# Optimization experiments

Measured on AMD Instinct MI355X. Metric: run time of the kernel, lower is better.

Reference implementation:

```python
import jax, jax.numpy as jnp
import numpy as np

N_EMBED = 512
E_DIM = 256
BETA = 0.25


def setup_inputs() -> dict:
    key = jax.random.key(0)
    k1, k2 = jax.random.split(key)
    z = jax.random.normal(k1, (32, 16, 16, 16, E_DIM), dtype=jnp.float32)
    embedding = jax.random.normal(k2, (N_EMBED, E_DIM), dtype=jnp.float32)
    return {"z": z, "embedding": embedding}


def reference(z, embedding):
    # Flatten spatial/batch dims: [N, e_dim]
    zf = z.reshape(-1, E_DIM)
    # similarity = ||z||^2 + ||e||^2 - 2 z.e  (squared distances)
    sim = (
        jnp.sum(zf * zf, axis=1, keepdims=True)
        + jnp.sum(embedding * embedding, axis=1)
        - 2.0 * jnp.einsum("bd,nd->bn", zf, embedding)
    )
    # NOTE: original code uses argmax (farthest code) -- faithfully reproduced.
    codebook_idxs = jnp.argmax(sim, axis=-1)
    # histogram side-effect: codebook_hist[idx] += 1
    hist = jnp.zeros((N_EMBED,), dtype=jnp.float32).at[codebook_idxs].add(1.0)
    z_q = embedding[codebook_idxs].reshape(z.shape)
    vq_loss = jnp.mean((z_q - jax.lax.stop_gradient(z)) ** 2)
    commitment_loss = BETA * jnp.mean((jax.lax.stop_gradient(z_q) - z) ** 2)
    # straight-through estimator
    z_q_st = z + jax.lax.stop_gradient(z_q - z)
    return (z_q_st, vq_loss, commitment_loss, codebook_idxs, hist)
```

## Files before the change

kernel.cpp:

```cpp
#include <hip/hip_runtime.h>
#include <hip/hip_bf16.h>

#define D 256
#define NC 512
#define NROWS 131072L

#define OFF_ZQ   0L
#define OFF_VQ   33554432L
#define OFF_CM   33554433L
#define OFF_IDX  33554434L
#define OFF_HIST 33685506L

#define WS_LPART 0
#define WS_HIST  2048
#define WS_E2    2560
#define WS_CNT   3072
#define WS_AMB   3136
#define WS_FIDX  134208
#define WS_BK    265280
#define WS_NEED  (330816L * 4)

#define MARGIN 1.25f

typedef __attribute__((ext_vector_type(8))) short bf16x8;
typedef __attribute__((ext_vector_type(4))) float f32x4;

#define AS1 __attribute__((address_space(1)))
#define AS3 __attribute__((address_space(3)))

__device__ __forceinline__ unsigned short f2bf(float f) {
    union { float f; unsigned int u; } a; a.f = f;
    return (unsigned short)((a.u + 0x7FFFu + ((a.u >> 16) & 1u)) >> 16);
}

__global__ void vq_init(float* __restrict__ ws) {
    int i = blockIdx.x * 1024 + threadIdx.x;
    if (i < 3073) ws[i] = 0.0f;
}

__global__ void vq_e2(const float* __restrict__ e, float* __restrict__ e2) {
    int c = blockIdx.x;
    int l = threadIdx.x;
    float4 v = *(const float4*)(e + c * D + l * 4);
    float s = v.x * v.x + v.y * v.y + v.z * v.z + v.w * v.w;
    #pragma unroll
    for (int off = 32; off; off >>= 1) s += __shfl_xor(s, off);
    if (l == 0) e2[c] = s;
}

__global__ void vq_convB(const float* __restrict__ e, unsigned short* __restrict__ Bk) {
    int code = blockIdx.x, k = threadIdx.x;
    unsigned short h = f2bf(e[code * D + k]);
    Bk[((k >> 5) * NC + code) * 32 + (k & 31)] = h;
}

__global__ __launch_bounds__(512, 4)
void vq_gemm(const float* __restrict__ z, const unsigned short* __restrict__ Bk,
             const float* __restrict__ e2, int* __restrict__ fidx,
             int* __restrict__ acnt, int* __restrict__ alist) {
    __shared__ __align__(16) unsigned short zh[64 * 264];
    __shared__ __align__(16) unsigned short Bs[512 * 32];
    __shared__ float red[64 * 4 * 3];

    const int tid = threadIdx.x;
    const int w = tid >> 6, l = tid & 63, q = l >> 4, ln = l & 15;
    const int wm = w >> 2, wn = w & 3;
    const long row0 = (long)blockIdx.x * 64;

    #pragma unroll
    for (int j = 0; j < 8; ++j) {
        int c = j * 512 + tid;
        int row = c >> 6, c4 = (c & 63) * 4;
        float4 av = *(const float4*)(z + (row0 + row) * D + c4);
        *(ushort4*)&zh[row * 264 + c4] =
            make_ushort4(f2bf(av.x), f2bf(av.y), f2bf(av.z), f2bf(av.w));
    }

    int bidx[8];
    #pragma unroll
    for (int nt = 0; nt < 8; ++nt) {
        int code = wn * 128 + nt * 16 + ln;
        int c = code * 4 + q;
        int d = c ^ ((code >> 1) & 3);
        bidx[nt] = d * 8;
    }

    f32x4 acc[2][8];
    #pragma unroll
    for (int mt = 0; mt < 2; ++mt)
        #pragma unroll
        for (int nt = 0; nt < 8; ++nt) acc[mt][nt] = (f32x4){0.f, 0.f, 0.f, 0.f};

    for (int s = 0; s < 8; ++s) {
        __syncthreads();
        const unsigned short* slabB = Bk + s * (NC * 32);
        #pragma unroll
        for (int j = 0; j < 4; ++j) {
            int dd = j * 512 + tid;
            int cc = dd ^ ((dd >> 3) & 3);
            __builtin_amdgcn_global_load_lds((const AS1 void*)(slabB + cc * 8),
                                             (AS3 void*)(Bs + dd * 8), 16, 0, 0);
        }
        __syncthreads();
        bf16x8 af[2], bfr[8];
        #pragma unroll
        for (int mt = 0; mt < 2; ++mt)
            af[mt] = *(const bf16x8*)&zh[(wm * 32 + mt * 16 + ln) * 264 + s * 32 + q * 8];
        #pragma unroll
        for (int nt = 0; nt < 8; ++nt)
            bfr[nt] = *(const bf16x8*)&Bs[bidx[nt]];
        #pragma unroll
        for (int mt = 0; mt < 2; ++mt)
            #pragma unroll
            for (int nt = 0; nt < 8; ++nt)
                acc[mt][nt] = __builtin_amdgcn_mfma_f32_16x16x32_bf16(af[mt], bfr[nt], acc[mt][nt], 0, 0, 0);
    }

    float e2v[8];
    #pragma unroll
    for (int nt = 0; nt < 8; ++nt) e2v[nt] = e2[wn * 128 + nt * 16 + ln];

    #pragma unroll
    for (int mt = 0; mt < 2; ++mt) {
        #pragma unroll
        for (int r = 0; r < 4; ++r) {
            float v1 = -3.0e38f, v2 = -3.0e38f; int i1 = 0;
            #pragma unroll
            for (int nt = 0; nt < 8; ++nt) {
                float v = e2v[nt] - 2.0f * acc[mt][nt][r];
                int c = wn * 128 + nt * 16 + ln;
                if (v > v1) { v2 = v1; v1 = v; i1 = c; }
                else if (v > v2) v2 = v;
            }
            #pragma unroll
            for (int off = 1; off < 16; off <<= 1) {
                float ov1 = __shfl_xor(v1, off);
                float ov2 = __shfl_xor(v2, off);
                int   oi1 = __shfl_xor(i1, off);
                if (ov1 > v1 || (ov1 == v1 && oi1 < i1)) {
                    v2 = fmaxf(v1, ov2); v1 = ov1; i1 = oi1;
                } else {
                    v2 = fmaxf(v2, ov1);
                }
            }
            if (ln == 0) {
                int rr = wm * 32 + mt * 16 + q * 4 + r;
                red[rr * 12 + wn * 3 + 0] = v1;
                red[rr * 12 + wn * 3 + 1] = (float)i1;
                red[rr * 12 + wn * 3 + 2] = v2;
            }
        }
    }
    __syncthreads();
    if (tid < 64) {
        float v1 = -3.0e38f, v2 = -3.0e38f; int i1 = 0;
        #pragma unroll
        for (int g = 0; g < 4; ++g) {
            float rv1 = red[tid * 12 + g * 3 + 0];
            int   ri  = (int)red[tid * 12 + g * 3 + 1];
            float rv2 = red[tid * 12 + g * 3 + 2];
            if (rv1 > v1) { v2 = fmaxf(v1, rv2); v1 = rv1; i1 = ri; }
            else v2 = fmaxf(v2, rv1);
        }
        fidx[row0 + tid] = i1;
        if (v1 - v2 < MARGIN) {
            int ppos = atomicAdd(acnt, 1);
            alist[ppos] = (int)(row0 + tid);
        }
    }
}

__global__ __launch_bounds__(256, 2)
void vq_refine(const float* __restrict__ z, const float* __restrict__ e,
               const float* __restrict__ e2, const int* __restrict__ acnt,
               const int* __restrict__ alist, int* __restrict__ fidx) {
    __shared__ __align__(16) float z_s[32][D];
    __shared__ __align__(16) float e_s[16][NC + 4];
    __shared__ int rowg[32];
    __shared__ int idx_s[32];
    const int tid = threadIdx.x, lane = tid & 63, w = tid >> 6;
    const int cnt = *acnt;
    for (int g = blockIdx.x; g * 32 < cnt; g += gridDim.x) {
        const int base = g * 32;
        __syncthreads();
        if (tid < 32) rowg[tid] = alist[min(base + tid, cnt - 1)];
        __syncthreads();
        #pragma unroll
        for (int j = 0; j < 8; ++j) {
            int c = j * 256 + tid, rl = c >> 6, c4 = (c & 63) * 4;
            *(float4*)&z_s[rl][c4] = *(const float4*)(z + (long)rowg[rl] * D + c4);
        }
        float acc[8][8];
        #pragma unroll
        for (int r = 0; r < 8; ++r)
            #pragma unroll
            for (int c = 0; c < 8; ++c) acc[r][c] = 0.0f;
        const int r0 = w * 8, c_lo = lane * 4;
        for (int kc = 0; kc < D; kc += 16) {
            __syncthreads();
            #pragma unroll
            for (int p = 0; p < 8; ++p) {
                int c = p * 64 + (tid >> 2), kk4 = (tid & 3) * 4;
                float4 v = *(const float4*)(e + c * D + kc + kk4);
                e_s[kk4 + 0][c] = v.x; e_s[kk4 + 1][c] = v.y;
                e_s[kk4 + 2][c] = v.z; e_s[kk4 + 3][c] = v.w;
            }
            __syncthreads();
            #pragma unroll
            for (int k4 = 0; k4 < 16; k4 += 4) {
                float zr[8][4];
                #pragma unroll
                for (int r = 0; r < 8; ++r) *(float4*)zr[r] = *(const float4*)&z_s[r0 + r][kc + k4];
                #pragma unroll
                for (int kk = 0; kk < 4; ++kk) {
                    float ev[8];
                    *(float4*)&ev[0] = *(const float4*)&e_s[k4 + kk][c_lo];
                    *(float4*)&ev[4] = *(const float4*)&e_s[k4 + kk][c_lo + 256];
                    #pragma unroll
                    for (int r = 0; r < 8; ++r)
                        #pragma unroll
                        for (int c = 0; c < 8; ++c) acc[r][c] = fmaf(zr[r][kk], ev[c], acc[r][c]);
                }
            }
        }
        float e2v[8];
        #pragma unroll
        for (int gg = 0; gg < 2; ++gg)
            #pragma unroll
            for (int i = 0; i < 4; ++i) e2v[gg * 4 + i] = e2[gg * 256 + c_lo + i];
        #pragma unroll
        for (int r = 0; r < 8; ++r) {
            float bvv = -3.0e38f; int bc = 0;
            #pragma unroll
            for (int c = 0; c < 8; ++c) {
                int col = (c >> 2) * 256 + c_lo + (c & 3);
                float v = e2v[c] - 2.0f * acc[r][c];
                if (v > bvv) { bvv = v; bc = col; }
            }
            #pragma unroll
            for (int off = 32; off; off >>= 1) {
                float ov = __shfl_xor(bvv, off); int oc = __shfl_xor(bc, off);
                if (ov > bvv || (ov == bvv && oc < bc)) { bvv = ov; bc = oc; }
            }
            if (lane == 0) idx_s[r0 + r] = bc;
        }
        __syncthreads();
        if (tid < 32 && base + tid < cnt) fidx[rowg[tid]] = idx_s[tid];
    }
}

__global__ __launch_bounds__(256)
void vq_hist(const int* __restrict__ fidx, float* __restrict__ out,
             float* __restrict__ hist) {
    __shared__ int h[NC];
    const int t = threadIdx.x;
    h[t] = 0; h[t + 256] = 0;
    __syncthreads();
    const long base = (long)blockIdx.x * 2048;
    #pragma unroll
    for (int j = 0; j < 8; ++j) {
        long i = base + j * 256 + t;
        int idx = fidx[i];
        out[OFF_IDX + i] = (float)idx;
        atomicAdd(&h[idx], 1);
    }
    __syncthreads();
    #pragma unroll
    for (int j = 0; j < 2; ++j) {
        int k = j * 256 + t;
        int c = h[k];
        if (c) atomicAdd(&hist[k], (float)c);
    }
}

__global__ __launch_bounds__(256)
void vq_epi(const float* __restrict__ z, const float* __restrict__ e,
            const int* __restrict__ fidx, float* __restrict__ out,
            float* __restrict__ lpart) {
    __shared__ int idxs[64];
    __shared__ float rs[4];
    const int t = threadIdx.x, lane = t & 63, w = t >> 6;
    const long row0 = (long)blockIdx.x * 64;
    if (t < 64) idxs[t] = fidx[row0 + t];
    __syncthreads();
    float ls = 0.f;
    #pragma unroll 4
    for (int j = 0; j < 16; ++j) {
        const int r = w * 16 + j;
        const long row = row0 + r;
        const int idx = idxs[r];
        float4 zv = *(const float4*)(z + row * D + lane * 4);
        float4 ev = *(const float4*)(e + (long)idx * D + lane * 4);
        float4 dq;
        dq.x = ev.x - zv.x; dq.y = ev.y - zv.y; dq.z = ev.z - zv.z; dq.w = ev.w - zv.w;
        float4 o;
        o.x = zv.x + dq.x; o.y = zv.y + dq.y; o.z = zv.z + dq.z; o.w = zv.w + dq.w;
        *(float4*)(out + OFF_ZQ + row * D + lane * 4) = o;
        ls += dq.x * dq.x + dq.y * dq.y + dq.z * dq.z + dq.w * dq.w;
    }
    #pragma unroll
    for (int off = 32; off; off >>= 1) ls += __shfl_xor(ls, off);
    if (lane == 0) rs[w] = ls;
    __syncthreads();
    if (t == 0) lpart[blockIdx.x] = rs[0] + rs[1] + rs[2] + rs[3];
}

__global__ void vq_fin(const float* __restrict__ ws, float* __restrict__ out) {
    __shared__ float sred[16];
    const int t = threadIdx.x, lane = t & 63, w = t >> 6;
    float s = ws[WS_LPART + t] + ws[WS_LPART + t + 1024];
    #pragma unroll
    for (int off = 32; off; off >>= 1) s += __shfl_xor(s, off);
    if (lane == 0) sred[w] = s;
    __syncthreads();
    if (t == 0) {
        float tot = 0.f;
        #pragma unroll
        for (int i = 0; i < 16; ++i) tot += sred[i];
        float m = tot / 33554432.0f;
        out[OFF_VQ] = m;
        out[OFF_CM] = 0.25f * m;
    }
    if (t < NC) out[OFF_HIST + t] = ws[WS_HIST + t];
}

__global__ __launch_bounds__(256, 2)
void vq_main_fb(const float* __restrict__ z, const float* __restrict__ e,
                const float* __restrict__ e2, float* __restrict__ out,
                float* __restrict__ ws_loss, float* __restrict__ ws_hist) {
    __shared__ __align__(16) float z_s[32][D];
    __shared__ __align__(16) float e_s[16][NC + 4];
    __shared__ int   idx_s[32];
    __shared__ float red_s[4];
    const int tid = threadIdx.x, lane = tid & 63, w = tid >> 6;
    const long row0 = (long)blockIdx.x * 32;
    {
        const float4* zg = (const float4*)(z + row0 * D);
        float4* zs = (float4*)(&z_s[0][0]);
        #pragma unroll
        for (int i = 0; i < 8; ++i) zs[i * 256 + tid] = zg[i * 256 + tid];
    }
    float acc[8][8];
    #pragma unroll
    for (int r = 0; r < 8; ++r)
        #pragma unroll
        for (int c = 0; c < 8; ++c) acc[r][c] = 0.0f;
    const int r0 = w * 8, c_lo = lane * 4;
    for (int kc = 0; kc < D; kc += 16) {
        __syncthreads();
        #pragma unroll
        for (int p = 0; p < 8; ++p) {
            int c = p * 64 + (tid >> 2), kk4 = (tid & 3) * 4;
            float4 v = *(const float4*)(e + c * D + kc + kk4);
            e_s[kk4 + 0][c] = v.x; e_s[kk4 + 1][c] = v.y;
            e_s[kk4 + 2][c] = v.z; e_s[kk4 + 3][c] = v.w;
        }
        __syncthreads();
        #pragma unroll
        for (int k4 = 0; k4 < 16; k4 += 4) {
            float zr[8][4];
            #pragma unroll
            for (int r = 0; r < 8; ++r) *(float4*)zr[r] = *(const float4*)&z_s[r0 + r][kc + k4];
            #pragma unroll
            for (int kk = 0; kk < 4; ++kk) {
                float ev[8];
                *(float4*)&ev[0] = *(const float4*)&e_s[k4 + kk][c_lo];
                *(float4*)&ev[4] = *(const float4*)&e_s[k4 + kk][c_lo + 256];
                #pragma unroll
                for (int r = 0; r < 8; ++r)
                    #pragma unroll
                    for (int c = 0; c < 8; ++c) acc[r][c] = fmaf(zr[r][kk], ev[c], acc[r][c]);
            }
        }
    }
    float e2v[8];
    #pragma unroll
    for (int g = 0; g < 2; ++g)
        #pragma unroll
        for (int i = 0; i < 4; ++i) e2v[g * 4 + i] = e2[g * 256 + c_lo + i];
    #pragma unroll
    for (int r = 0; r < 8; ++r) {
        float bvv = -3.0e38f; int bc = 0;
        #pragma unroll
        for (int c = 0; c < 8; ++c) {
            int col = (c >> 2) * 256 + c_lo + (c & 3);
            float v = e2v[c] - 2.0f * acc[r][c];
            if (v > bvv) { bvv = v; bc = col; }
        }
        #pragma unroll
        for (int off = 32; off; off >>= 1) {
            float ov = __shfl_xor(bvv, off); int oc = __shfl_xor(bc, off);
            if (ov > bvv || (ov == bvv && oc < bc)) { bvv = ov; bc = oc; }
        }
        if (lane == 0) idx_s[r0 + r] = bc;
    }
    __syncthreads();
    if (tid < 32) {
        int bc = idx_s[tid];
        out[OFF_IDX + row0 + tid] = (float)bc;
        atomicAdd(&ws_hist[bc], 1.0f);
    }
    float lsum = 0.0f;
    for (int r = 0; r < 32; ++r) {
        int idx = idx_s[r];
        float ev = e[idx * D + tid];
        float zv = z_s[r][tid];
        float dq = ev - zv;
        out[OFF_ZQ + (row0 + r) * D + tid] = zv + dq;
        lsum += dq * dq;
    }
    #pragma unroll
    for (int off = 32; off; off >>= 1) lsum += __shfl_xor(lsum, off);
    if (lane == 0) red_s[w] = lsum;
    __syncthreads();
    if (tid == 0) atomicAdd(ws_loss, red_s[0] + red_s[1] + red_s[2] + red_s[3]);
}

__global__ void vq_init_fb(float* __restrict__ ws) {
    int t = threadIdx.x;
    if (t < 513) ws[t] = 0.0f;
}
__global__ void vq_fin_fb(const float* __restrict__ ws, float* __restrict__ out) {
    int t = blockIdx.x * blockDim.x + threadIdx.x;
    if (t < NC) out[OFF_HIST + t] = ws[1 + t];
    if (t == NC) {
        float m = ws[0] / 33554432.0f;
        out[OFF_VQ] = m; out[OFF_CM] = 0.25f * m;
    }
}

extern "C" void kernel_launch(void* const* d_in, const int* in_sizes, int n_in,
                              void* d_out, int out_size, void* d_ws, size_t ws_size,
                              hipStream_t stream) {
    const float* z = (const float*)d_in[0];
    const float* e = (const float*)d_in[1];
    float* out = (float*)d_out;
    float* ws  = (float*)d_ws;

    if (ws_size >= (size_t)WS_NEED) {
        float* lpart = ws + WS_LPART;
        float* hist  = ws + WS_HIST;
        float* e2    = ws + WS_E2;
        int*   acnt  = (int*)(ws + WS_CNT);
        int*   alist = (int*)(ws + WS_AMB);
        int*   fidx  = (int*)(ws + WS_FIDX);
        unsigned short* Bk = (unsigned short*)(ws + WS_BK);

        vq_init<<<4, 1024, 0, stream>>>(ws);
        vq_e2<<<NC, 64, 0, stream>>>(e, e2);
        vq_convB<<<NC, 256, 0, stream>>>(e, Bk);
        vq_gemm<<<2048, 512, 0, stream>>>(z, Bk, e2, fidx, acnt, alist);
        vq_refine<<<512, 256, 0, stream>>>(z, e, e2, acnt, alist, fidx);
        vq_hist<<<64, 256, 0, stream>>>(fidx, out, hist);
        vq_epi<<<2048, 256, 0, stream>>>(z, e, fidx, out, lpart);
        vq_fin<<<1, 1024, 0, stream>>>(ws, out);
    } else {
        float* ws_loss = ws;
        float* ws_hist = ws + 1;
        float* ws_e2   = ws + 513;
        vq_init_fb<<<1, 1024, 0, stream>>>(ws);
        vq_e2<<<NC, 64, 0, stream>>>(e, ws_e2);
        vq_main_fb<<<4096, 256, 0, stream>>>(z, e, ws_e2, out, ws_loss, ws_hist);
        vq_fin_fb<<<3, 256, 0, stream>>>(ws, out);
    }
}
```

Baseline: 390.0 us.

## Read codebook directly from global in GEMM and fuse e2 into convB

The GEMM kernel no longer stages codebook slabs into LDS with global_load_lds and two barriers per k-step. Each wave now owns 64 codes across all 64 rows (a 4x4 MFMA tile) and loads B fragments straight from global/L2, which removes the per-slab barriers and LDS traffic. The reduction buffer grows to 8 waves per row, padded to stride 25. Separately, the codebook squared norms are computed inside the bf16 conversion kernel, saving one launch. The risk is more L2 traffic and latency per wave because there is no LDS reuse of B across waves.

Result: slower. 402.5 us (+3.2%).

```diff
diff --git a/kernel.cpp b/kernel.cpp
--- a/kernel.cpp
+++ b/kernel.cpp
@@ -48,10 +48,18 @@
     if (l == 0) e2[c] = s;
 }
 
-__global__ void vq_convB(const float* __restrict__ e, unsigned short* __restrict__ Bk) {
+__global__ void vq_convB(const float* __restrict__ e, unsigned short* __restrict__ Bk,
+                         float* __restrict__ e2) {
+    __shared__ float r4[4];
     int code = blockIdx.x, k = threadIdx.x;
-    unsigned short h = f2bf(e[code * D + k]);
-    Bk[((k >> 5) * NC + code) * 32 + (k & 31)] = h;
+    float v = e[code * D + k];
+    Bk[((k >> 5) * NC + code) * 32 + (k & 31)] = f2bf(v);
+    float s = v * v;
+    #pragma unroll
+    for (int off = 32; off; off >>= 1) s += __shfl_xor(s, off);
+    if ((k & 63) == 0) r4[k >> 6] = s;
+    __syncthreads();
+    if (k == 0) e2[code] = r4[0] + r4[1] + r4[2] + r4[3];
 }
 
 __global__ __launch_bounds__(512, 4)
@@ -59,12 +67,10 @@
              const float* __restrict__ e2, int* __restrict__ fidx,
              int* __restrict__ acnt, int* __restrict__ alist) {
     __shared__ __align__(16) unsigned short zh[64 * 264];
-    __shared__ __align__(16) unsigned short Bs[512 * 32];
-    __shared__ float red[64 * 4 * 3];
+    __shared__ float red[64 * 25];
 
     const int tid = threadIdx.x;
     const int w = tid >> 6, l = tid & 63, q = l >> 4, ln = l & 15;
-    const int wm = w >> 2, wn = w & 3;
     const long row0 = (long)blockIdx.x * 64;
 
     #pragma unroll
@@ -75,60 +81,47 @@
         *(ushort4*)&zh[row * 264 + c4] =
             make_ushort4(f2bf(av.x), f2bf(av.y), f2bf(av.z), f2bf(av.w));
     }
-
-    int bidx[8];
-    #pragma unroll
-    for (int nt = 0; nt < 8; ++nt) {
-        int code = wn * 128 + nt * 16 + ln;
-        int c = code * 4 + q;
-        int d = c ^ ((code >> 1) & 3);
-        bidx[nt] = d * 8;
-    }
-
-    f32x4 acc[2][8];
-    #pragma unroll
-    for (int mt = 0; mt < 2; ++mt)
-        #pragma unroll
-        for (int nt = 0; nt < 8; ++nt) acc[mt][nt] = (f32x4){0.f, 0.f, 0.f, 0.f};
-
+    __syncthreads();
+
+    const unsigned short* bbase = Bk + ((w * 64 + ln) * 32 + q * 8);
+    const unsigned short* abase = &zh[ln * 264 + q * 8];
+
+    f32x4 acc[4][4];
+    #pragma unroll
+    for (int mt = 0; mt < 4; ++mt)
+        #pragma unroll
+        for (int nt = 0; nt < 4; ++nt) acc[mt][nt] = (f32x4){0.f, 0.f, 0.f, 0.f};
+
+    #pragma unroll
     for (int s = 0; s < 8; ++s) {
-        __syncthreads();
-        const unsigned short* slabB = Bk + s * (NC * 32);
-        #pragma unroll
-        for (int j = 0; j < 4; ++j) {
-            int dd = j * 512 + tid;
-            int cc = dd ^ ((dd >> 3) & 3);
-            __builtin_amdgcn_global_load_lds((const AS1 void*)(slabB + cc * 8),
-                                             (AS3 void*)(Bs + dd * 8), 16, 0, 0);
-        }
-        __syncthreads();
-        bf16x8 af[2], bfr[8];
-        #pragma unroll
-        for (int mt = 0; mt < 2; ++mt)
-            af[mt] = *(const bf16x8*)&zh[(wm * 32 + mt * 16 + ln) * 264 + s * 32 + q * 8];
-        #pragma unroll
-        for (int nt = 0; nt < 8; ++nt)
-            bfr[nt] = *(const bf16x8*)&Bs[bidx[nt]];
-        #pragma unroll
-        for (int mt = 0; mt < 2; ++mt)
-            #pragma unroll
-            for (int nt = 0; nt < 8; ++nt)
+        const unsigned short* bs = bbase + s * (NC * 32);
+        bf16x8 bfr[4], af[4];
+        #pragma unroll
+        for (int nt = 0; nt < 4; ++nt)
+            bfr[nt] = *(const bf16x8*)(bs + nt * (16 * 32));
+        #pragma unroll
+        for (int mt = 0; mt < 4; ++mt)
+            af[mt] = *(const bf16x8*)(abase + mt * (16 * 264) + s * 32);
+        #pragma unroll
+        for (int mt = 0; mt < 4; ++mt)
+            #pragma unroll
+            for (int nt = 0; nt < 4; ++nt)
                 acc[mt][nt] = __builtin_amdgcn_mfma_f32_16x16x32_bf16(af[mt], bfr[nt], acc[mt][nt], 0, 0, 0);
     }
 
-    float e2v[8];
-    #pragma unroll
-    for (int nt = 0; nt < 8; ++nt) e2v[nt] = e2[wn * 128 + nt * 16 + ln];
-
-    #pragma unroll
-    for (int mt = 0; mt < 2; ++mt) {
+    float e2v[4];
+    #pragma unroll
+    for (int nt = 0; nt < 4; ++nt) e2v[nt] = e2[w * 64 + nt * 16 + ln];
+
+    #pragma unroll
+    for (int mt = 0; mt < 4; ++mt) {
         #pragma unroll
         for (int r = 0; r < 4; ++r) {
             float v1 = -3.0e38f, v2 = -3.0e38f; int i1 = 0;
             #pragma unroll
-            for (int nt = 0; nt < 8; ++nt) {
+            for (int nt = 0; nt < 4; ++nt) {
                 float v = e2v[nt] - 2.0f * acc[mt][nt][r];
-                int c = wn * 128 + nt * 16 + ln;
+                int c = w * 64 + nt * 16 + ln;
                 if (v > v1) { v2 = v1; v1 = v; i1 = c; }
                 else if (v > v2) v2 = v;
             }
@@ -144,10 +137,10 @@
                 }
             }
             if (ln == 0) {
-                int rr = wm * 32 + mt * 16 + q * 4 + r;
-                red[rr * 12 + wn * 3 + 0] = v1;
-                red[rr * 12 + wn * 3 + 1] = (float)i1;
-                red[rr * 12 + wn * 3 + 2] = v2;
+                int rr = mt * 16 + q * 4 + r;
+                red[rr * 25 + w * 3 + 0] = v1;
+                red[rr * 25 + w * 3 + 1] = (float)i1;
+                red[rr * 25 + w * 3 + 2] = v2;
             }
         }
     }
@@ -155,10 +148,10 @@
     if (tid < 64) {
         float v1 = -3.0e38f, v2 = -3.0e38f; int i1 = 0;
         #pragma unroll
-        for (int g = 0; g < 4; ++g) {
-            float rv1 = red[tid * 12 + g * 3 + 0];
-            int   ri  = (int)red[tid * 12 + g * 3 + 1];
-            float rv2 = red[tid * 12 + g * 3 + 2];
+        for (int g = 0; g < 8; ++g) {
+            float rv1 = red[tid * 25 + g * 3 + 0];
+            int   ri  = (int)red[tid * 25 + g * 3 + 1];
+            float rv2 = red[tid * 25 + g * 3 + 2];
             if (rv1 > v1) { v2 = fmaxf(v1, rv2); v1 = rv1; i1 = ri; }
             else v2 = fmaxf(v2, rv1);
         }
@@ -447,8 +440,7 @@
         unsigned short* Bk = (unsigned short*)(ws + WS_BK);
 
         vq_init<<<4, 1024, 0, stream>>>(ws);
-        vq_e2<<<NC, 64, 0, stream>>>(e, e2);
-        vq_convB<<<NC, 256, 0, stream>>>(e, Bk);
+        vq_convB<<<NC, 256, 0, stream>>>(e, Bk, e2);
         vq_gemm<<<2048, 512, 0, stream>>>(z, Bk, e2, fidx, acnt, alist);
         vq_refine<<<512, 256, 0, stream>>>(z, e, e2, acnt, alist, fidx);
         vq_hist<<<64, 256, 0, stream>>>(fidx, out, hist);
```
